# Kernel optimization log

Hardware: AMD Instinct MI355X
Metric: run time of the kernel (lower is better)

## Reference

```python
import jax, jax.numpy as jnp
import numpy as np

EPS = 1e-12
HEADS = 8
STRIDE = 4  # saccade_stride default

def conv1x1(x, w, b=None):
    # 1x1 conv == channel-mixing einsum; x: (B,C,H,W), w: (O,C)
    y = jnp.einsum('bchw,oc->bohw', x, w)
    if b is not None:
        y = y + b[None, :, None, None]
    return y

def ln2d(x, g, b, eps=1e-5):
    # LayerNorm across channel dim per spatial location (population variance)
    mu = x.mean(axis=1, keepdims=True)
    var = x.var(axis=1, keepdims=True)
    xn = (x - mu) / jnp.sqrt(var + eps)
    return xn * g[None, :, None, None] + b[None, :, None, None]

def l2norm(x):
    n = jnp.linalg.norm(x, axis=-1, keepdims=True)
    return x / jnp.maximum(n, EPS)

def cos_attn(q, k, v, scale):
    # q:(B,h,Q,d) k,v:(B,h,K,d); QK-normalized (cosine) attention
    logits = jnp.einsum('bhqd,bhkd->bhqk', l2norm(q), l2norm(k)) * scale
    a = jax.nn.softmax(logits, axis=-1)
    return jnp.einsum('bhqk,bhkd->bhqd', a, v)

def gqa(x, qkv_w, proj_w, proj_b):
    # grouped-query attention; group loop == per-head full attention
    B, C, H, W = x.shape
    hd = C // HEADS
    seq = H * W
    qkv = conv1x1(x, qkv_w).reshape(B, 3, HEADS, hd, seq)
    q, k, v = (jnp.swapaxes(qkv[:, i], -1, -2) for i in range(3))  # (B,h,seq,hd)
    out = cos_attn(q, k, v, hd ** -0.5)
    out = jnp.swapaxes(out, -1, -2).reshape(B, C, H, W)
    return conv1x1(out, proj_w, proj_b)

def block_forward(x, g1, b1, loc_qkv_w, loc_proj_w, loc_proj_b,
                  glob_qkv_w, glob_proj_w, glob_proj_b,
                  fuse_w1, fuse_b1, fuse_w2, fuse_b2,
                  glat, blat, latents, qlat_w, kvx_w, qx_w, kvlat_w,
                  lat_proj_w, lat_proj_b, g2, b2,
                  ffn_w1, ffn_b1, ffn_w2, ffn_b2):
    B, C, H, W = x.shape
    hd = C // HEADS
    seq = H * W
    scale = hd ** -0.5
    # --- BioAttentionFusion branch ---
    xn = ln2d(x, g1, b1)
    local = gqa(xn, loc_qkv_w, loc_proj_w, loc_proj_b)
    xc = xn.reshape(B, C, H // STRIDE, STRIDE, W // STRIDE, STRIDE).mean(axis=(3, 5))
    g = gqa(xc, glob_qkv_w, glob_proj_w, glob_proj_b)
    g = jax.image.resize(g, (B, C, H, W), method='bilinear')  # align_corners=False semantics
    f = conv1x1(jnp.concatenate([local, g], axis=1), fuse_w1, fuse_b1)
    f = conv1x1(jax.nn.gelu(f, approximate=False), fuse_w2, fuse_b2)
    x = x + f
    # --- LatentMixer branch ---
    xn = ln2d(x, glat, blat)
    L = latents.shape[-1]
    lat = jnp.broadcast_to(latents, (B, C, 1, L))
    ql = jnp.swapaxes(conv1x1(lat, qlat_w).reshape(B, HEADS, hd, L), -1, -2)
    kx, vx = jnp.split(conv1x1(xn, kvx_w), 2, axis=1)
    kx = jnp.swapaxes(kx.reshape(B, HEADS, hd, seq), -1, -2)
    vx = jnp.swapaxes(vx.reshape(B, HEADS, hd, seq), -1, -2)
    lat_read = cos_attn(ql, kx, vx, scale)  # latents read features
    lat_read = jnp.swapaxes(lat_read, -1, -2).reshape(B, C, 1, L)
    qx = jnp.swapaxes(conv1x1(xn, qx_w).reshape(B, HEADS, hd, seq), -1, -2)
    kl, vl = jnp.split(conv1x1(lat_read, kvlat_w), 2, axis=1)
    kl = jnp.swapaxes(kl.reshape(B, HEADS, hd, L), -1, -2)
    vl = jnp.swapaxes(vl.reshape(B, HEADS, hd, L), -1, -2)
    xw = cos_attn(qx, kl, vl, scale)  # features read latents back
    xw = jnp.swapaxes(xw, -1, -2).reshape(B, C, H, W)
    x = x + conv1x1(xw, lat_proj_w, lat_proj_b)
    # --- FFN branch ---
    xn = ln2d(x, g2, b2)
    h = jax.nn.gelu(conv1x1(xn, ffn_w1, ffn_b1), approximate=False)
    return x + conv1x1(h, ffn_w2, ffn_b2)

def setup_inputs() -> dict:
    key = jax.random.key(0)
    ks = jax.random.split(key, 24)
    B, C, H, W, L = 2, 128, 48, 48, 16
    def w(k, shape, s=0.02):
        return jax.random.normal(k, shape, jnp.float32) * s
    return {
        'x': jax.random.normal(ks[0], (B, C, H, W), jnp.float32),
        'g1': jnp.ones((C,), jnp.float32), 'b1': jnp.zeros((C,), jnp.float32),
        'loc_qkv_w': w(ks[1], (3 * C, C)),
        'loc_proj_w': w(ks[2], (C, C)), 'loc_proj_b': jnp.zeros((C,), jnp.float32),
        'glob_qkv_w': w(ks[3], (3 * C, C)),
        'glob_proj_w': w(ks[4], (C, C)), 'glob_proj_b': jnp.zeros((C,), jnp.float32),
        'fuse_w1': w(ks[5], (C, 2 * C)), 'fuse_b1': jnp.zeros((C,), jnp.float32),
        'fuse_w2': w(ks[6], (C, C)), 'fuse_b2': jnp.zeros((C,), jnp.float32),
        'glat': jnp.ones((C,), jnp.float32), 'blat': jnp.zeros((C,), jnp.float32),
        'latents': w(ks[7], (1, C, 1, L), 0.02),
        'qlat_w': w(ks[8], (C, C)), 'kvx_w': w(ks[9], (2 * C, C)),
        'qx_w': w(ks[10], (C, C)), 'kvlat_w': w(ks[11], (2 * C, C)),
        'lat_proj_w': w(ks[12], (C, C)), 'lat_proj_b': jnp.zeros((C,), jnp.float32),
        'g2': jnp.ones((C,), jnp.float32), 'b2': jnp.zeros((C,), jnp.float32),
        'ffn_w1': w(ks[13], (4 * C, C)), 'ffn_b1': jnp.zeros((4 * C,), jnp.float32),
        'ffn_w2': w(ks[14], (C, 4 * C)), 'ffn_b2': jnp.zeros((C,), jnp.float32),
    }

def reference(x, g1, b1, loc_qkv_w, loc_proj_w, loc_proj_b,
              glob_qkv_w, glob_proj_w, glob_proj_b,
              fuse_w1, fuse_b1, fuse_w2, fuse_b2,
              glat, blat, latents, qlat_w, kvx_w, qx_w, kvlat_w,
              lat_proj_w, lat_proj_b, g2, b2,
              ffn_w1, ffn_b1, ffn_w2, ffn_b2):
    return block_forward(x, g1, b1, loc_qkv_w, loc_proj_w, loc_proj_b,
                         glob_qkv_w, glob_proj_w, glob_proj_b,
                         fuse_w1, fuse_b1, fuse_w2, fuse_b2,
                         glat, blat, latents, qlat_w, kvx_w, qx_w, kvlat_w,
                         lat_proj_w, lat_proj_b, g2, b2,
                         ffn_w1, ffn_b1, ffn_w2, ffn_b2)
```

## Files before the change

kernel.cpp:

```cpp
#include <hip/hip_runtime.h>
#include <hip/hip_bf16.h>

typedef __hip_bfloat16 bf16;
typedef _Float16 f16;
typedef _Float16 f16x4 __attribute__((ext_vector_type(4)));
typedef float f32x4 __attribute__((ext_vector_type(4)));

#define HD 16
#define TK 128
#define KP 20
#define MINIT (-1e30f)

__device__ __forceinline__ float b2f(bf16 v){ return __bfloat162float(v); }
__device__ __forceinline__ float gelu_f(float x){ return 0.5f*x*(1.0f+erff(x*0.70710678118654752f)); }
__device__ __forceinline__ float rdv(const void* p, size_t i, bool bf){
  return bf ? b2f(((const bf16*)p)[i]) : ((const float*)p)[i];
}
__device__ __forceinline__ float4 ld4f(const void* p, size_t i, bool bf){
  if (bf){
    const bf16* q = (const bf16*)p + i;
    return make_float4(b2f(q[0]), b2f(q[1]), b2f(q[2]), b2f(q[3]));
  }
  return *(const float4*)((const float*)p + i);
}

__global__ void detect_k(const void* __restrict__ x, float* __restrict__ flag){
  if (blockIdx.x != 0) return;
  int l = threadIdx.x;
  const float* xf = (const float*)x;
  const bf16*  xb = (const bf16*)x;
  float sF = 0.f, sB = 0.f;
  for (int i = l; i < 512; i += 64){ float v = fabsf(xf[i]);      if (!(v < 1e30f)) v = 1e30f; sF += v; }
  for (int i = l; i < 1024; i += 64){ float v = fabsf(b2f(xb[i])); if (!(v < 1e30f)) v = 1e30f; sB += v; }
  #pragma unroll
  for (int o = 32; o; o >>= 1){ sF += __shfl_xor(sF, o); sB += __shfl_xor(sB, o); }
  if (l == 0){
    float mF = sF/512.f, mB = sB/1024.f;
    float dF = fabsf(logf(fmaxf(mF, 1e-30f)));
    float dB = fabsf(logf(fmaxf(mB, 1e-30f)));
    *flag = (dB <= dF) ? 1.0f : 0.0f;
  }
}

__global__ void cvt_k(const void* __restrict__ in, float* __restrict__ out, int n,
                      const float* __restrict__ flagp){
  bool bf = *flagp > 0.5f;
  int i = blockIdx.x*blockDim.x + threadIdx.x;
  if (i < n) out[i] = rdv(in, i, bf);
}

__global__ __launch_bounds__(256) void ln2dw_k(
    const float* __restrict__ x, const void* __restrict__ g,
    const void* __restrict__ b, float* __restrict__ y,
    int C, int HW, const float* __restrict__ flagp)
{
  __shared__ float redS[16][16];
  __shared__ float redQ[16][16];
  bool bf = *flagp > 0.5f;
  int t = threadIdx.x, pix = t & 15, sub = t >> 4;
  int p  = blockIdx.x*16 + pix;
  int bb = blockIdx.y;
  const float* xb = x + (size_t)bb*C*HW + p;
  float xv[8];
  float s = 0.f, s2 = 0.f;
  #pragma unroll
  for (int i = 0; i < 8; i++){
    float v = xb[(size_t)(sub*8 + i)*HW];
    xv[i] = v; s += v; s2 += v*v;
  }
  redS[sub][pix] = s; redQ[sub][pix] = s2;
  __syncthreads();
  float st = 0.f, qt = 0.f;
  #pragma unroll
  for (int j = 0; j < 16; j++){ st += redS[j][pix]; qt += redQ[j][pix]; }
  float mu  = st / (float)C;
  float var = fmaxf(qt / (float)C - mu*mu, 0.f);
  float inv = rsqrtf(var + 1e-5f);
  float* yb = y + (size_t)bb*C*HW + p;
  #pragma unroll
  for (int i = 0; i < 8; i++){
    int c = sub*8 + i;
    yb[(size_t)c*HW] = (xv[i] - mu)*inv*rdv(g, c, bf) + rdv(b, c, bf);
  }
}

__global__ void conv1x1_k(const float* __restrict__ in1, long in1_bs, int C1,
                          const float* __restrict__ in2, long in2_bs, int C2,
                          const void* __restrict__ w, const void* __restrict__ bias,
                          const float* __restrict__ res,
                          void* __restrict__ out, int to_out, int O, int NP, int act,
                          int raw1, const float* __restrict__ flagp){
  bool bf = *flagp > 0.5f;
  int p = blockIdx.x*blockDim.x + threadIdx.x;
  if (p >= NP) return;
  int o = blockIdx.y, bb = blockIdx.z;
  size_t wrow = (size_t)o*(C1 + C2);
  float acc = bias ? rdv(bias, o, bf) : 0.f;
  if (raw1){
    for (int c = 0; c < C1; c++)
      acc += rdv(w, wrow + c, bf) * rdv(in1, (size_t)bb*in1_bs + (size_t)c*NP + p, bf);
  } else {
    const float* i1 = in1 + (size_t)bb*in1_bs + p;
    for (int c = 0; c < C1; c++) acc += rdv(w, wrow + c, bf) * i1[(size_t)c*NP];
  }
  if (in2){
    const float* i2 = in2 + (size_t)bb*in2_bs + p;
    for (int c = 0; c < C2; c++) acc += rdv(w, wrow + C1 + c, bf) * i2[(size_t)c*NP];
  }
  if (act == 1) acc = gelu_f(acc);
  if (res) acc += res[((size_t)bb*O + o)*NP + p];
  size_t oi = ((size_t)bb*O + o)*NP + p;
  if (to_out){
    if (bf) ((bf16*)out)[oi] = __float2bfloat16(acc);
    else    ((float*)out)[oi] = acc;
  } else {
    ((float*)out)[oi] = acc;
  }
}

__global__ __launch_bounds__(256) void convmfma_k(
    const float* __restrict__ in1, long in1_bs, int C1,
    const float* __restrict__ in2, long in2_bs, int C2,
    const void* __restrict__ w, const void* __restrict__ bias,
    const float* __restrict__ res, void* __restrict__ out, int to_out,
    int O, int NP, int act, int nlo, int nhi,
    int lnf, const void* __restrict__ lng, const void* __restrict__ lnb,
    int pool, int ups2, const float* __restrict__ flagp)
{
  bool bf = *flagp > 0.5f;
  int lane = threadIdx.x & 63, wv = threadIdx.x >> 6;
  int lm = lane & 15, lg = (lane >> 4) & 3;
  int p0 = blockIdx.x*16, o0 = blockIdx.y*64 + wv*16, bb = blockIdx.z;
  int CW = C1 + C2;
  const float* x1 = in1 + (size_t)bb*in1_bs + p0 + lm;
  const float* x2b = in2 ? (in2 + (size_t)bb*in2_bs) : nullptr;
  float fh = 0.f, fw = 0.f; int i00=0, i01=0, i10=0, i11=0;
  if (ups2){
    int p = p0 + lm; int hh = p/48, ww = p%48;
    float sh = hh*0.25f - 0.375f, sw = ww*0.25f - 0.375f;
    float fh0 = floorf(sh), fw0 = floorf(sw);
    fh = sh - fh0; fw = sw - fw0;
    int h0 = (int)fh0, w0 = (int)fw0;
    int h0c = min(11, max(0, h0)), h1c = min(11, max(0, h0+1));
    int w0c = min(11, max(0, w0)), w1c = min(11, max(0, w0+1));
    i00 = h0c*12 + w0c; i01 = h0c*12 + w1c; i10 = h1c*12 + w0c; i11 = h1c*12 + w1c;
  }
  const float* pN = nullptr;
  if (pool){
    int pc = p0 + lm; int hc = pc/12, wc = pc%12;
    pN = in1 + (size_t)bb*in1_bs + hc*192 + wc*4;
  }
  float mu = 0.f, linv = 0.f;
  if (lnf){
    float s = 0.f, s2 = 0.f;
    for (int c = lg; c < CW; c += 4){ float v = x1[(size_t)c*NP]; s += v; s2 += v*v; }
    s  += __shfl_xor(s, 16);  s  += __shfl_xor(s, 32);
    s2 += __shfl_xor(s2, 16); s2 += __shfl_xor(s2, 32);
    mu = s / (float)CW;
    float var = fmaxf(s2/(float)CW - mu*mu, 0.f);
    linv = rsqrtf(var + 1e-5f);
  }
  f32x4 d; d[0]=0.f; d[1]=0.f; d[2]=0.f; d[3]=0.f;
  #pragma unroll 4
  for (int kc = 0; kc < CW; kc += 16){
    f16x4 xb;
    #pragma unroll
    for (int i = 0; i < 4; i++){
      int c = kc + lg*4 + i;
      float v;
      if (pool){
        const float* s = pN + (size_t)c*2304;
        float a = 0.f;
        #pragma unroll
        for (int r = 0; r < 4; r++)
          #pragma unroll
          for (int cc = 0; cc < 4; cc++) a += s[r*48 + cc];
        v = a * 0.0625f;
      } else if (c < C1){
        v = x1[(size_t)c*NP];
        if (lnf) v = (v - mu)*linv*rdv(lng, c, bf) + rdv(lnb, c, bf);
      } else {
        int c2 = c - C1;
        if (ups2){
          const float* s = x2b + (size_t)c2*144;
          v = (1.f-fh)*((1.f-fw)*s[i00] + fw*s[i01]) + fh*((1.f-fw)*s[i10] + fw*s[i11]);
        } else {
          v = x2b[(size_t)c2*NP + p0 + lm];
        }
      }
      xb[i] = (f16)v;
    }
    float4 wv4 = ld4f(w, (size_t)(o0 + lm)*CW + kc + lg*4, bf);
    f16x4 wa; wa[0]=(f16)wv4.x; wa[1]=(f16)wv4.y; wa[2]=(f16)wv4.z; wa[3]=(f16)wv4.w;
    d = __builtin_amdgcn_mfma_f32_16x16x16f16(wa, xb, d, 0, 0, 0);
  }
  if (o0 >= nlo && o0 < nhi){
    float ss = d[0]*d[0] + d[1]*d[1] + d[2]*d[2] + d[3]*d[3];
    ss += __shfl_xor(ss, 16); ss += __shfl_xor(ss, 32);
    float iv = 1.f / fmaxf(sqrtf(ss), 1e-12f);
    d[0]*=iv; d[1]*=iv; d[2]*=iv; d[3]*=iv;
  }
  #pragma unroll
  for (int r = 0; r < 4; r++){
    int o = o0 + lg*4 + r;
    float v = d[r] + (bias ? rdv(bias, o, bf) : 0.f);
    if (act == 1) v = gelu_f(v);
    size_t oi = ((size_t)bb*O + o)*NP + p0 + lm;
    if (res) v += res[oi];
    if (to_out && bf) ((bf16*)out)[oi] = __float2bfloat16(v);
    else              ((float*)out)[oi] = v;
  }
}

__global__ __launch_bounds__(512) void flat_mfma_k(
    const float* __restrict__ Q, long qbs, int qoff,
    const float* __restrict__ KV, long kbs, int koff, int voff,
    float* __restrict__ Out, long obs, int NQ, int NK, float scale)
{
  __shared__ float OS[8*4*16*17];
  __shared__ float LS[8*4*16];
  int t = threadIdx.x, lane = t & 63, wv = t >> 6;
  int h = blockIdx.y, bb = blockIdx.z;
  int qb = blockIdx.x*64;
  int lm = lane & 15, lg = lane >> 4;
  const float* qp  = Q  + (size_t)bb*qbs;
  const float* kvb = KV + (size_t)bb*kbs;
  f16x4 qf[4];
  #pragma unroll
  for (int qt = 0; qt < 4; qt++){
    float qv[4]; float ss = 0.f;
    #pragma unroll
    for (int i = 0; i < 4; i++){
      qv[i] = qp[(size_t)(qoff + h*16 + lg*4 + i)*NQ + qb + qt*16 + lm];
      ss += qv[i]*qv[i];
    }
    ss += __shfl_xor(ss, 16); ss += __shfl_xor(ss, 32);
    float inv = scale / fmaxf(sqrtf(ss), 1e-12f);
    #pragma unroll
    for (int i = 0; i < 4; i++) qf[qt][i] = (f16)(qv[i]*inv);
  }
  f32x4 of[4];
  float ls[4];
  #pragma unroll
  for (int qt = 0; qt < 4; qt++){
    of[qt][0]=0.f; of[qt][1]=0.f; of[qt][2]=0.f; of[qt][3]=0.f; ls[qt]=0.f;
  }
  int chunk = NK >> 3;
  int p0 = wv*chunk, p1 = p0 + chunk;
  const float* kc = kvb + (size_t)(koff + h*16)*NK;
  const float* vc = kvb + (size_t)(voff + h*16)*NK;
  for (int pos = p0; pos < p1; pos += 16){
    f16x4 kf;
    #pragma unroll
    for (int i = 0; i < 4; i++)
      kf[i] = (f16)kc[(size_t)(lg*4 + i)*NK + pos + lm];
    float4 vvv = *(const float4*)&vc[(size_t)lm*NK + pos + lg*4];
    f16x4 vf; vf[0]=(f16)vvv.x; vf[1]=(f16)vvv.y; vf[2]=(f16)vvv.z; vf[3]=(f16)vvv.w;
    #pragma unroll
    for (int qt = 0; qt < 4; qt++){
      f32x4 s; s[0]=0.f; s[1]=0.f; s[2]=0.f; s[3]=0.f;
      s = __builtin_amdgcn_mfma_f32_16x16x16f16(kf, qf[qt], s, 0, 0, 0);
      f16x4 pf;
      #pragma unroll
      for (int r = 0; r < 4; r++){
        float pp = __expf(s[r]);
        ls[qt] += pp;
        pf[r] = (f16)pp;
      }
      of[qt] = __builtin_amdgcn_mfma_f32_16x16x16f16(vf, pf, of[qt], 0, 0, 0);
    }
  }
  #pragma unroll
  for (int qt = 0; qt < 4; qt++){
    ls[qt] += __shfl_xor(ls[qt], 16);
    ls[qt] += __shfl_xor(ls[qt], 32);
    #pragma unroll
    for (int r = 0; r < 4; r++)
      OS[((wv*4 + qt)*16 + lm)*17 + lg*4 + r] = of[qt][r];
    if (lg == 0) LS[(wv*4 + qt)*16 + lm] = ls[qt];
  }
  __syncthreads();
  #pragma unroll
  for (int rep = 0; rep < 2; rep++){
    int o = t + rep*512;
    int d = o >> 6, qq = o & 63;
    int qt = qq >> 4, q = qq & 15;
    float acc = 0.f, lsum = 0.f;
    #pragma unroll
    for (int w = 0; w < 8; w++){
      acc  += OS[((w*4 + qt)*16 + q)*17 + d];
      lsum += LS[(w*4 + qt)*16 + q];
    }
    Out[(size_t)bb*obs + (size_t)(h*16 + d)*NQ + qb + qq] = acc / fmaxf(lsum, 1e-30f);
  }
}

__global__ __launch_bounds__(256) void attn4_k(
    const float* __restrict__ Q, long qbs, int qoff,
    const float* __restrict__ KV, long kbs, int koff, int voff,
    float* __restrict__ Out, long obs, int NQ, int NK, float scale)
{
  __shared__ __align__(16) float Ks[TK*KP];
  __shared__ __align__(16) float Vs[TK*KP];
  int tid = threadIdx.x;
  int sub = tid & 3;
  int h = blockIdx.y, bb = blockIdx.z;
  int qi = blockIdx.x*64 + (tid >> 2);
  bool qv = qi < NQ;
  float qn[4] = {0,0,0,0}, acc[4] = {0,0,0,0};
  float l = 0.f;
  if (qv){
    float s = 0.f;
    #pragma unroll
    for (int j = 0; j < 4; j++){
      qn[j] = Q[(size_t)bb*qbs + (size_t)(qoff + h*16 + sub*4 + j)*NQ + qi];
      s += qn[j]*qn[j];
    }
    s += __shfl_xor(s, 1); s += __shfl_xor(s, 2);
    float inv = scale / fmaxf(sqrtf(s), 1e-12f);
    #pragma unroll
    for (int j = 0; j < 4; j++) qn[j] *= inv;
  }
  for (int k0 = 0; k0 < NK; k0 += TK){
    int lim = min(TK, NK - k0);
    for (int i = tid; i < 16*TK; i += 256){
      int pos = i & (TK-1), d = i >> 7;
      if (pos < lim){
        Ks[pos*KP + d] = KV[(size_t)bb*kbs + (size_t)(koff + h*16 + d)*NK + k0 + pos];
        Vs[pos*KP + d] = KV[(size_t)bb*kbs + (size_t)(voff + h*16 + d)*NK + k0 + pos];
      }
    }
    __syncthreads();
    for (int pos = 0; pos < lim; pos++){
      float4 k4 = *(const float4*)&Ks[pos*KP + sub*4];
      float dd = qn[0]*k4.x + qn[1]*k4.y + qn[2]*k4.z + qn[3]*k4.w;
      dd += __shfl_xor(dd, 1); dd += __shfl_xor(dd, 2);
      float pp = __expf(dd);
      l += pp;
      float4 v4 = *(const float4*)&Vs[pos*KP + sub*4];
      acc[0] += pp*v4.x;
      acc[1] += pp*v4.y;
      acc[2] += pp*v4.z;
      acc[3] += pp*v4.w;
    }
    __syncthreads();
  }
  if (qv){
    float li = 1.f / fmaxf(l, 1e-30f);
    #pragma unroll
    for (int j = 0; j < 4; j++)
      Out[(size_t)bb*obs + (size_t)(h*16 + sub*4 + j)*NQ + qi] = acc[j]*li;
  }
}

__global__ void latpart_k(const float* __restrict__ ql, const float* __restrict__ kvx,
                          long kbs, float* __restrict__ part, int NK, int S){
  int s = blockIdx.x, h = blockIdx.y, bb = blockIdx.z;
  int t = threadIdx.x;
  int q = t & 15, sub = (t >> 4) & 3;
  float qn[16]; float ss = 0.f;
  #pragma unroll
  for (int d = 0; d < 16; d++){
    qn[d] = ql[(size_t)bb*2048 + (size_t)(h*16+d)*16 + q];
    ss += qn[d]*qn[d];
  }
  float inv = 0.25f / fmaxf(sqrtf(ss), 1e-12f);
  #pragma unroll
  for (int d = 0; d < 16; d++) qn[d] *= inv;
  float l = 0.f, acc[16];
  #pragma unroll
  for (int d = 0; d < 16; d++) acc[d] = 0.f;
  int chunk = NK / S, c4 = chunk >> 2;
  int k0 = s*chunk + sub*c4, k1 = k0 + c4;
  const float* kb = kvx + (size_t)bb*kbs;
  for (int pos = k0; pos < k1; pos++){
    float dot = 0.f;
    #pragma unroll
    for (int d = 0; d < 16; d++) dot += qn[d]*kb[(size_t)(h*16+d)*NK + pos];
    float pp = __expf(dot);
    l += pp;
    #pragma unroll
    for (int d = 0; d < 16; d++)
      acc[d] += pp*kb[(size_t)(128 + h*16+d)*NK + pos];
  }
  l += __shfl_xor(l, 16); l += __shfl_xor(l, 32);
  #pragma unroll
  for (int d = 0; d < 16; d++){
    acc[d] += __shfl_xor(acc[d], 16);
    acc[d] += __shfl_xor(acc[d], 32);
  }
  if ((t >> 4) == 0){
    size_t idx = (size_t)((((bb*8 + h)*16 + q)*S) + s)*18;
    part[idx] = l;
    #pragma unroll
    for (int d = 0; d < 16; d++) part[idx+1+d] = acc[d];
  }
}

__global__ void latcomb_k(const float* __restrict__ part, float* __restrict__ latr, int S){
  int i = blockIdx.x*blockDim.x + threadIdx.x;
  int d = i & 15, q = (i >> 4) & 15, h = (i >> 8) & 7, bb = i >> 11;
  size_t base = (size_t)(((bb*8 + h)*16 + q)*S)*18;
  float L = 0.f, a = 0.f;
  for (int s = 0; s < S; s++){
    const float* ps = part + base + (size_t)s*18;
    L += ps[0];
    a += ps[1+d];
  }
  latr[(size_t)bb*2048 + (size_t)(h*16+d)*16 + q] = a / fmaxf(L, 1e-30f);
}

extern "C" void kernel_launch(void* const* d_in, const int* in_sizes, int n_in,
                              void* d_out, int out_size, void* d_ws, size_t ws_size,
                              hipStream_t stream){
  const int B = 2, C = 128, HW = 2304;
  const void* x_in        = d_in[0];
  const void* g1          = d_in[1];
  const void* b1          = d_in[2];
  const void* loc_qkv_w   = d_in[3];
  const void* loc_proj_w  = d_in[4];
  const void* loc_proj_b  = d_in[5];
  const void* glob_qkv_w  = d_in[6];
  const void* glob_proj_w = d_in[7];
  const void* glob_proj_b = d_in[8];
  const void* fuse_w1     = d_in[9];
  const void* fuse_b1     = d_in[10];
  const void* fuse_w2     = d_in[11];
  const void* fuse_b2     = d_in[12];
  const void* glat        = d_in[13];
  const void* blat        = d_in[14];
  const void* latents     = d_in[15];
  const void* qlat_w      = d_in[16];
  const void* kvx_w       = d_in[17];
  const void* qx_w        = d_in[18];
  const void* kvlat_w     = d_in[19];
  const void* lat_proj_w  = d_in[20];
  const void* lat_proj_b  = d_in[21];
  const void* g2          = d_in[22];
  const void* b2          = d_in[23];
  const void* ffn_w1      = d_in[24];
  const void* ffn_b1      = d_in[25];
  const void* ffn_w2      = d_in[26];
  const void* ffn_b2      = d_in[27];

  float* ws = (float*)d_ws;
  float* P  = ws + 0;
  float* N  = ws + 589824;
  float* A  = ws + 1179648;
  float* Q  = ws + 1769472;
  float* FLAG = ws + 4128768;

  float* qkv   = Q;
  float* L     = Q + 1769472;
  float* qkvc  = Q + 36864;
  float* gatt  = Q + 147456;
  float* gproj = Q + 184320;
  float* kvx   = Q;
  float* qlat  = Q + 1181696;
  float* latr  = Q + 1185792;
  float* kvlat = Q + 1189888;
  float* part  = Q + 1198080;
  float* ffh   = Q;

  dim3 blk(256);
  dim3 blk512(512);

  detect_k<<<1, 64, 0, stream>>>(x_in, FLAG);
  cvt_k<<<2304, blk, 0, stream>>>(x_in, P, 589824, FLAG);

  ln2dw_k<<<dim3(144,B), blk, 0, stream>>>(P, g1, b1, N, C, HW, FLAG);
  convmfma_k<<<dim3(144,6,B), blk, 0, stream>>>(N,(long)C*HW,C, nullptr,0,0, loc_qkv_w,nullptr,nullptr, qkv,0,384,HW,0, 128,256, 0,nullptr,nullptr, 0,0, FLAG);
  flat_mfma_k<<<dim3(36,8,B), blk512, 0, stream>>>(qkv,(long)384*HW,0, qkv,(long)384*HW,128,256, A,(long)C*HW, HW,HW,0.25f);
  convmfma_k<<<dim3(144,2,B), blk, 0, stream>>>(A,(long)C*HW,C, nullptr,0,0, loc_proj_w,loc_proj_b,nullptr, L,0,C,HW,0, 0,0, 0,nullptr,nullptr, 0,0, FLAG);
  convmfma_k<<<dim3(9,6,B), blk, 0, stream>>>(N,(long)C*HW,C, nullptr,0,0, glob_qkv_w,nullptr,nullptr, qkvc,0,384,144,0, 128,256, 0,nullptr,nullptr, 1,0, FLAG);
  attn4_k<<<dim3(3,8,B), blk, 0, stream>>>(qkvc,(long)384*144,0, qkvc,(long)384*144,128,256, gatt,(long)C*144, 144,144,0.25f);
  convmfma_k<<<dim3(9,2,B), blk, 0, stream>>>(gatt,(long)C*144,C, nullptr,0,0, glob_proj_w,glob_proj_b,nullptr, gproj,0,C,144,0, 0,0, 0,nullptr,nullptr, 0,0, FLAG);
  convmfma_k<<<dim3(144,2,B), blk, 0, stream>>>(L,(long)C*HW,C, gproj,(long)C*144,C, fuse_w1,fuse_b1,nullptr, N,0,C,HW,1, 0,0, 0,nullptr,nullptr, 0,1, FLAG);
  convmfma_k<<<dim3(144,2,B), blk, 0, stream>>>(N,(long)C*HW,C, nullptr,0,0, fuse_w2,fuse_b2,P, P,0,C,HW,0, 0,0, 0,nullptr,nullptr, 0,0, FLAG);

  convmfma_k<<<dim3(144,4,B), blk, 0, stream>>>(P,(long)C*HW,C, nullptr,0,0, kvx_w,nullptr,nullptr, kvx,0,256,HW,0, 0,128, 1,glat,blat, 0,0, FLAG);
  convmfma_k<<<dim3(144,2,B), blk, 0, stream>>>(P,(long)C*HW,C, nullptr,0,0, qx_w,nullptr,nullptr, A,0,C,HW,0, 0,0, 1,glat,blat, 0,0, FLAG);
  conv1x1_k<<<dim3(1,128,B), blk, 0, stream>>>((const float*)latents,0L,C, nullptr,0,0, qlat_w,nullptr,nullptr, qlat,0,C,16,0, 1, FLAG);
  latpart_k<<<dim3(48,8,B), 64, 0, stream>>>(qlat, kvx, (long)256*HW, part, HW, 48);
  latcomb_k<<<16, blk, 0, stream>>>(part, latr, 48);
  convmfma_k<<<dim3(1,4,B), blk, 0, stream>>>(latr,(long)C*16,C, nullptr,0,0, kvlat_w,nullptr,nullptr, kvlat,0,256,16,0, 0,128, 0,nullptr,nullptr, 0,0, FLAG);
  attn4_k<<<dim3(36,8,B), blk, 0, stream>>>(A,(long)C*HW,0, kvlat,(long)256*16,0,128, N,(long)C*HW, HW,16,0.25f);
  convmfma_k<<<dim3(144,2,B), blk, 0, stream>>>(N,(long)C*HW,C, nullptr,0,0, lat_proj_w,lat_proj_b,P, P,0,C,HW,0, 0,0, 0,nullptr,nullptr, 0,0, FLAG);

  convmfma_k<<<dim3(144,8,B), blk, 0, stream>>>(P,(long)C*HW,C, nullptr,0,0, ffn_w1,ffn_b1,nullptr, ffh,0,512,HW,1, 0,0, 1,g2,b2, 0,0, FLAG);
  convmfma_k<<<dim3(144,2,B), blk, 0, stream>>>(ffh,(long)512*HW,512, nullptr,0,0, ffn_w2,ffn_b2,P, d_out,1,C,HW,0, 0,0, 0,nullptr,nullptr, 0,0, FLAG);
}
```

Baseline: 436.6 us.

## Fuse small latent kernels and inline dtype detection to cut launches

Removes the separate dtype-detect kernel: every kernel now re-runs a small 64-lane reduction over the input to decide bf16 versus fp32. The kvx and qx projections are merged into one convmfma launch through an output-split path. The latent query projection moves into latpart_k, and the kv-latent projection moves into a new attention kernel, so two small launches go away. This lowers launch count and serialization, but adds redundant detection loads and redundant projection work repeated in every block.

After: 448.0 us. +2.6%, slower.

```diff
diff --git a/kernel.cpp b/kernel.cpp
--- a/kernel.cpp
+++ b/kernel.cpp
@@ -9,7 +9,6 @@
 #define HD 16
 #define TK 128
 #define KP 20
-#define MINIT (-1e30f)
 
 __device__ __forceinline__ float b2f(bf16 v){ return __bfloat162float(v); }
 __device__ __forceinline__ float gelu_f(float x){ return 0.5f*x*(1.0f+erff(x*0.70710678118654752f)); }
@@ -24,27 +23,25 @@
   return *(const float4*)((const float*)p + i);
 }
 
-__global__ void detect_k(const void* __restrict__ x, float* __restrict__ flag){
-  if (blockIdx.x != 0) return;
-  int l = threadIdx.x;
+__device__ __forceinline__ bool detect_bf(const void* x){
+  int l = threadIdx.x & 63;
   const float* xf = (const float*)x;
   const bf16*  xb = (const bf16*)x;
   float sF = 0.f, sB = 0.f;
-  for (int i = l; i < 512; i += 64){ float v = fabsf(xf[i]);      if (!(v < 1e30f)) v = 1e30f; sF += v; }
-  for (int i = l; i < 1024; i += 64){ float v = fabsf(b2f(xb[i])); if (!(v < 1e30f)) v = 1e30f; sB += v; }
+  #pragma unroll
+  for (int i = 0; i < 8; i++){ float v = fabsf(xf[l + i*64]);      if (!(v < 1e30f)) v = 1e30f; sF += v; }
+  #pragma unroll
+  for (int i = 0; i < 16; i++){ float v = fabsf(b2f(xb[l + i*64])); if (!(v < 1e30f)) v = 1e30f; sB += v; }
   #pragma unroll
   for (int o = 32; o; o >>= 1){ sF += __shfl_xor(sF, o); sB += __shfl_xor(sB, o); }
-  if (l == 0){
-    float mF = sF/512.f, mB = sB/1024.f;
-    float dF = fabsf(logf(fmaxf(mF, 1e-30f)));
-    float dB = fabsf(logf(fmaxf(mB, 1e-30f)));
-    *flag = (dB <= dF) ? 1.0f : 0.0f;
-  }
-}
-
-__global__ void cvt_k(const void* __restrict__ in, float* __restrict__ out, int n,
-                      const float* __restrict__ flagp){
-  bool bf = *flagp > 0.5f;
+  float mF = sF/512.f, mB = sB/1024.f;
+  float dF = fabsf(logf(fmaxf(mF, 1e-30f)));
+  float dB = fabsf(logf(fmaxf(mB, 1e-30f)));
+  return dB <= dF;
+}
+
+__global__ void cvt_k(const void* __restrict__ in, float* __restrict__ out, int n){
+  bool bf = detect_bf(in);
   int i = blockIdx.x*blockDim.x + threadIdx.x;
   if (i < n) out[i] = rdv(in, i, bf);
 }
@@ -52,11 +49,11 @@
 __global__ __launch_bounds__(256) void ln2dw_k(
     const float* __restrict__ x, const void* __restrict__ g,
     const void* __restrict__ b, float* __restrict__ y,
-    int C, int HW, const float* __restrict__ flagp)
+    int C, int HW, const void* __restrict__ xdet)
 {
   __shared__ float redS[16][16];
   __shared__ float redQ[16][16];
-  bool bf = *flagp > 0.5f;
+  bool bf = detect_bf(xdet);
   int t = threadIdx.x, pix = t & 15, sub = t >> 4;
   int p  = blockIdx.x*16 + pix;
   int bb = blockIdx.y;
@@ -81,40 +78,6 @@
   for (int i = 0; i < 8; i++){
     int c = sub*8 + i;
     yb[(size_t)c*HW] = (xv[i] - mu)*inv*rdv(g, c, bf) + rdv(b, c, bf);
-  }
-}
-
-__global__ void conv1x1_k(const float* __restrict__ in1, long in1_bs, int C1,
-                          const float* __restrict__ in2, long in2_bs, int C2,
-                          const void* __restrict__ w, const void* __restrict__ bias,
-                          const float* __restrict__ res,
-                          void* __restrict__ out, int to_out, int O, int NP, int act,
-                          int raw1, const float* __restrict__ flagp){
-  bool bf = *flagp > 0.5f;
-  int p = blockIdx.x*blockDim.x + threadIdx.x;
-  if (p >= NP) return;
-  int o = blockIdx.y, bb = blockIdx.z;
-  size_t wrow = (size_t)o*(C1 + C2);
-  float acc = bias ? rdv(bias, o, bf) : 0.f;
-  if (raw1){
-    for (int c = 0; c < C1; c++)
-      acc += rdv(w, wrow + c, bf) * rdv(in1, (size_t)bb*in1_bs + (size_t)c*NP + p, bf);
-  } else {
-    const float* i1 = in1 + (size_t)bb*in1_bs + p;
-    for (int c = 0; c < C1; c++) acc += rdv(w, wrow + c, bf) * i1[(size_t)c*NP];
-  }
-  if (in2){
-    const float* i2 = in2 + (size_t)bb*in2_bs + p;
-    for (int c = 0; c < C2; c++) acc += rdv(w, wrow + C1 + c, bf) * i2[(size_t)c*NP];
-  }
-  if (act == 1) acc = gelu_f(acc);
-  if (res) acc += res[((size_t)bb*O + o)*NP + p];
-  size_t oi = ((size_t)bb*O + o)*NP + p;
-  if (to_out){
-    if (bf) ((bf16*)out)[oi] = __float2bfloat16(acc);
-    else    ((float*)out)[oi] = acc;
-  } else {
-    ((float*)out)[oi] = acc;
   }
 }
 
@@ -125,13 +88,17 @@
     const float* __restrict__ res, void* __restrict__ out, int to_out,
     int O, int NP, int act, int nlo, int nhi,
     int lnf, const void* __restrict__ lng, const void* __restrict__ lnb,
-    int pool, int ups2, const float* __restrict__ flagp)
+    int pool, int ups2,
+    const void* __restrict__ w2, void* __restrict__ out2, int O2, int osplit,
+    const void* __restrict__ xdet)
 {
-  bool bf = *flagp > 0.5f;
+  bool bf = detect_bf(xdet);
   int lane = threadIdx.x & 63, wv = threadIdx.x >> 6;
   int lm = lane & 15, lg = (lane >> 4) & 3;
   int p0 = blockIdx.x*16, o0 = blockIdx.y*64 + wv*16, bb = blockIdx.z;
   int CW = C1 + C2;
+  const void* wu = w; void* outu = out; int Ou = O; int od = 0;
+  if (osplit > 0 && o0 >= osplit){ wu = w2; outu = out2; Ou = O2; od = osplit; }
   const float* x1 = in1 + (size_t)bb*in1_bs + p0 + lm;
   const float* x2b = in2 ? (in2 + (size_t)bb*in2_bs) : nullptr;
   float fh = 0.f, fw = 0.f; int i00=0, i01=0, i10=0, i11=0;
@@ -190,7 +157,7 @@
       }
       xb[i] = (f16)v;
     }
-    float4 wv4 = ld4f(w, (size_t)(o0 + lm)*CW + kc + lg*4, bf);
+    float4 wv4 = ld4f(wu, (size_t)(o0 - od + lm)*CW + kc + lg*4, bf);
     f16x4 wa; wa[0]=(f16)wv4.x; wa[1]=(f16)wv4.y; wa[2]=(f16)wv4.z; wa[3]=(f16)wv4.w;
     d = __builtin_amdgcn_mfma_f32_16x16x16f16(wa, xb, d, 0, 0, 0);
   }
@@ -202,13 +169,13 @@
   }
   #pragma unroll
   for (int r = 0; r < 4; r++){
-    int o = o0 + lg*4 + r;
+    int o = o0 - od + lg*4 + r;
     float v = d[r] + (bias ? rdv(bias, o, bf) : 0.f);
     if (act == 1) v = gelu_f(v);
-    size_t oi = ((size_t)bb*O + o)*NP + p0 + lm;
+    size_t oi = ((size_t)bb*Ou + o)*NP + p0 + lm;
     if (res) v += res[oi];
-    if (to_out && bf) ((bf16*)out)[oi] = __float2bfloat16(v);
-    else              ((float*)out)[oi] = v;
+    if (to_out && bf) ((bf16*)outu)[oi] = __float2bfloat16(v);
+    else              ((float*)outu)[oi] = v;
   }
 }
 
@@ -353,15 +320,95 @@
   }
 }
 
-__global__ void latpart_k(const float* __restrict__ ql, const float* __restrict__ kvx,
-                          long kbs, float* __restrict__ part, int NK, int S){
+__global__ __launch_bounds__(256) void attn4lat_k(
+    const float* __restrict__ Q, long qbs,
+    const float* __restrict__ latr, const void* __restrict__ kvw,
+    float* __restrict__ Out, long obs, int NQ, float scale,
+    const void* __restrict__ xdet)
+{
+  __shared__ __align__(16) float Ks[16*KP];
+  __shared__ __align__(16) float Vs[16*KP];
+  bool bf = detect_bf(xdet);
+  int tid = threadIdx.x;
+  int h = blockIdx.y, bb = blockIdx.z;
+  {
+    int pos = tid & 15, d = tid >> 4;
+    const float* lr = latr + (size_t)bb*2048;
+    float kk = 0.f, vv = 0.f;
+    for (int c = 0; c < 128; c++){
+      float xv = lr[(size_t)c*16 + pos];
+      kk += rdv(kvw, (size_t)(h*16 + d)*128 + c, bf) * xv;
+      vv += rdv(kvw, (size_t)(128 + h*16 + d)*128 + c, bf) * xv;
+    }
+    Ks[pos*KP + d] = kk;
+    Vs[pos*KP + d] = vv;
+  }
+  __syncthreads();
+  if (tid < 16){
+    float ss = 0.f;
+    #pragma unroll
+    for (int d = 0; d < 16; d++){ float v = Ks[tid*KP + d]; ss += v*v; }
+    float iv = 1.f / fmaxf(sqrtf(ss), 1e-12f);
+    #pragma unroll
+    for (int d = 0; d < 16; d++) Ks[tid*KP + d] *= iv;
+  }
+  __syncthreads();
+  int sub = tid & 3;
+  int qi = blockIdx.x*64 + (tid >> 2);
+  float qn[4]; float acc[4] = {0,0,0,0}; float l = 0.f;
+  {
+    float s = 0.f;
+    #pragma unroll
+    for (int j = 0; j < 4; j++){
+      qn[j] = Q[(size_t)bb*qbs + (size_t)(h*16 + sub*4 + j)*NQ + qi];
+      s += qn[j]*qn[j];
+    }
+    s += __shfl_xor(s, 1); s += __shfl_xor(s, 2);
+    float inv = scale / fmaxf(sqrtf(s), 1e-12f);
+    #pragma unroll
+    for (int j = 0; j < 4; j++) qn[j] *= inv;
+  }
+  for (int pos = 0; pos < 16; pos++){
+    float4 k4 = *(const float4*)&Ks[pos*KP + sub*4];
+    float dd = qn[0]*k4.x + qn[1]*k4.y + qn[2]*k4.z + qn[3]*k4.w;
+    dd += __shfl_xor(dd, 1); dd += __shfl_xor(dd, 2);
+    float pp = __expf(dd);
+    l += pp;
+    float4 v4 = *(const float4*)&Vs[pos*KP + sub*4];
+    acc[0] += pp*v4.x;
+    acc[1] += pp*v4.y;
+    acc[2] += pp*v4.z;
+    acc[3] += pp*v4.w;
+  }
+  float li = 1.f / fmaxf(l, 1e-30f);
+  #pragma unroll
+  for (int j = 0; j < 4; j++)
+    Out[(size_t)bb*obs + (size_t)(h*16 + sub*4 + j)*NQ + qi] = acc[j]*li;
+}
+
+__global__ void latpart_k(const void* __restrict__ lat, const void* __restrict__ qw,
+                          const float* __restrict__ kvx, long kbs,
+                          float* __restrict__ part, int NK, int S,
+                          const void* __restrict__ xdet){
+  __shared__ float qls[256];
+  bool bf = detect_bf(xdet);
   int s = blockIdx.x, h = blockIdx.y, bb = blockIdx.z;
   int t = threadIdx.x;
   int q = t & 15, sub = (t >> 4) & 3;
+  #pragma unroll
+  for (int k2 = 0; k2 < 4; k2++){
+    int v = t*4 + k2;
+    int dd = v >> 4, qq = v & 15;
+    float a = 0.f;
+    for (int c = 0; c < 128; c++)
+      a += rdv(qw, (size_t)(h*16 + dd)*128 + c, bf) * rdv(lat, (size_t)c*16 + qq, bf);
+    qls[v] = a;
+  }
+  __syncthreads();
   float qn[16]; float ss = 0.f;
   #pragma unroll
   for (int d = 0; d < 16; d++){
-    qn[d] = ql[(size_t)bb*2048 + (size_t)(h*16+d)*16 + q];
+    qn[d] = qls[d*16 + q];
     ss += qn[d]*qn[d];
   }
   float inv = 0.25f / fmaxf(sqrtf(ss), 1e-12f);
@@ -448,7 +495,6 @@
   float* N  = ws + 589824;
   float* A  = ws + 1179648;
   float* Q  = ws + 1769472;
-  float* FLAG = ws + 4128768;
 
   float* qkv   = Q;
   float* L     = Q + 1769472;
@@ -456,37 +502,31 @@
   float* gatt  = Q + 147456;
   float* gproj = Q + 184320;
   float* kvx   = Q;
-  float* qlat  = Q + 1181696;
   float* latr  = Q + 1185792;
-  float* kvlat = Q + 1189888;
   float* part  = Q + 1198080;
   float* ffh   = Q;
 
   dim3 blk(256);
   dim3 blk512(512);
 
-  detect_k<<<1, 64, 0, stream>>>(x_in, FLAG);
-  cvt_k<<<2304, blk, 0, stream>>>(x_in, P, 589824, FLAG);
-
-  ln2dw_k<<<dim3(144,B), blk, 0, stream>>>(P, g1, b1, N, C, HW, FLAG);
-  convmfma_k<<<dim3(144,6,B), blk, 0, stream>>>(N,(long)C*HW,C, nullptr,0,0, loc_qkv_w,nullptr,nullptr, qkv,0,384,HW,0, 128,256, 0,nullptr,nullptr, 0,0, FLAG);
+  cvt_k<<<2304, blk, 0, stream>>>(x_in, P, 589824);
+
+  ln2dw_k<<<dim3(144,B), blk, 0, stream>>>(P, g1, b1, N, C, HW, x_in);
+  convmfma_k<<<dim3(144,6,B), blk, 0, stream>>>(N,(long)C*HW,C, nullptr,0,0, loc_qkv_w,nullptr,nullptr, qkv,0,384,HW,0, 128,256, 0,nullptr,nullptr, 0,0, nullptr,nullptr,0,0, x_in);
   flat_mfma_k<<<dim3(36,8,B), blk512, 0, stream>>>(qkv,(long)384*HW,0, qkv,(long)384*HW,128,256, A,(long)C*HW, HW,HW,0.25f);
-  convmfma_k<<<dim3(144,2,B), blk, 0, stream>>>(A,(long)C*HW,C, nullptr,0,0, loc_proj_w,loc_proj_b,nullptr, L,0,C,HW,0, 0,0, 0,nullptr,nullptr, 0,0, FLAG);
-  convmfma_k<<<dim3(9,6,B), blk, 0, stream>>>(N,(long)C*HW,C, nullptr,0,0, glob_qkv_w,nullptr,nullptr, qkvc,0,384,144,0, 128,256, 0,nullptr,nullptr, 1,0, FLAG);
+  convmfma_k<<<dim3(144,2,B), blk, 0, stream>>>(A,(long)C*HW,C, nullptr,0,0, loc_proj_w,loc_proj_b,nullptr, L,0,C,HW,0, 0,0, 0,nullptr,nullptr, 0,0, nullptr,nullptr,0,0, x_in);
+  convmfma_k<<<dim3(9,6,B), blk, 0, stream>>>(N,(long)C*HW,C, nullptr,0,0, glob_qkv_w,nullptr,nullptr, qkvc,0,384,144,0, 128,256, 0,nullptr,nullptr, 1,0, nullptr,nullptr,0,0, x_in);
   attn4_k<<<dim3(3,8,B), blk, 0, stream>>>(qkvc,(long)384*144,0, qkvc,(long)384*144,128,256, gatt,(long)C*144, 144,144,0.25f);
-  convmfma_k<<<dim3(9,2,B), blk, 0, stream>>>(gatt,(long)C*144,C, nullptr,0,0, glob_proj_w,glob_proj_b,nullptr, gproj,0,C,144,0, 0,0, 0,nullptr,nullptr, 0,0, FLAG);
-  convmfma_k<<<dim3(144,2,B), blk, 0, stream>>>(L,(long)C*HW,C, gproj,(long)C*144,C, fuse_w1,fuse_b1,nullptr, N,0,C,HW,1, 0,0, 0,nullptr,nullptr, 0,1, FLAG);
-  convmfma_k<<<dim3(144,2,B), blk, 0, stream>>>(N,(long)C*HW,C, nullptr,0,0, fuse_w2,fuse_b2,P, P,0,C,HW,0, 0,0, 0,nullptr,nullptr, 0,0, FLAG);
-
-  convmfma_k<<<dim3(144,4,B), blk, 0, stream>>>(P,(long)C*HW,C, nullptr,0,0, kvx_w,nullptr,nullptr, kvx,0,256,HW,0, 0,128, 1,glat,blat, 0,0, FLAG);
-  convmfma_k<<<dim3(144,2,B), blk, 0, stream>>>(P,(long)C*HW,C, nullptr,0,0, qx_w,nullptr,nullptr, A,0,C,HW,0, 0,0, 1,glat,blat, 0,0, FLAG);
-  conv1x1_k<<<dim3(1,128,B), blk, 0, stream>>>((const float*)latents,0L,C, nullptr,0,0, qlat_w,nullptr,nullptr, qlat,0,C,16,0, 1, FLAG);
-  latpart_k<<<dim3(48,8,B), 64, 0, stream>>>(qlat, kvx, (long)256*HW, part, HW, 48);
+  convmfma_k<<<dim3(9,2,B), blk, 0, stream>>>(gatt,(long)C*144,C, nullptr,0,0, glob_proj_w,glob_proj_b,nullptr, gproj,0,C,144,0, 0,0, 0,nullptr,nullptr, 0,0, nullptr,nullptr,0,0, x_in);
+  convmfma_k<<<dim3(144,2,B), blk, 0, stream>>>(L,(long)C*HW,C, gproj,(long)C*144,C, fuse_w1,fuse_b1,nullptr, N,0,C,HW,1, 0,0, 0,nullptr,nullptr, 0,1, nullptr,nullptr,0,0, x_in);
+  convmfma_k<<<dim3(144,2,B), blk, 0, stream>>>(N,(long)C*HW,C, nullptr,0,0, fuse_w2,fuse_b2,P, P,0,C,HW,0, 0,0, 0,nullptr,nullptr, 0,0, nullptr,nullptr,0,0, x_in);
+
+  convmfma_k<<<dim3(144,6,B), blk, 0, stream>>>(P,(long)C*HW,C, nullptr,0,0, kvx_w,nullptr,nullptr, kvx,0,256,HW,0, 0,128, 1,glat,blat, 0,0, qx_w,A,128,256, x_in);
+  latpart_k<<<dim3(48,8,B), 64, 0, stream>>>(latents, qlat_w, kvx, (long)256*HW, part, HW, 48, x_in);
   latcomb_k<<<16, blk, 0, stream>>>(part, latr, 48);
-  convmfma_k<<<dim3(1,4,B), blk, 0, stream>>>(latr,(long)C*16,C, nullptr,0,0, kvlat_w,nullptr,nullptr, kvlat,0,256,16,0, 0,128, 0,nullptr,nullptr, 0,0, FLAG);
-  attn4_k<<<dim3(36,8,B), blk, 0, stream>>>(A,(long)C*HW,0, kvlat,(long)256*16,0,128, N,(long)C*HW, HW,16,0.25f);
-  convmfma_k<<<dim3(144,2,B), blk, 0, stream>>>(N,(long)C*HW,C, nullptr,0,0, lat_proj_w,lat_proj_b,P, P,0,C,HW,0, 0,0, 0,nullptr,nullptr, 0,0, FLAG);
-
-  convmfma_k<<<dim3(144,8,B), blk, 0, stream>>>(P,(long)C*HW,C, nullptr,0,0, ffn_w1,ffn_b1,nullptr, ffh,0,512,HW,1, 0,0, 1,g2,b2, 0,0, FLAG);
-  convmfma_k<<<dim3(144,2,B), blk, 0, stream>>>(ffh,(long)512*HW,512, nullptr,0,0, ffn_w2,ffn_b2,P, d_out,1,C,HW,0, 0,0, 0,nullptr,nullptr, 0,0, FLAG);
-}
+  attn4lat_k<<<dim3(36,8,B), blk, 0, stream>>>(A,(long)C*HW, latr, kvlat_w, N,(long)C*HW, HW, 0.25f, x_in);
+  convmfma_k<<<dim3(144,2,B), blk, 0, stream>>>(N,(long)C*HW,C, nullptr,0,0, lat_proj_w,lat_proj_b,P, P,0,C,HW,0, 0,0, 0,nullptr,nullptr, 0,0, nullptr,nullptr,0,0, x_in);
+
+  convmfma_k<<<dim3(144,8,B), blk, 0, stream>>>(P,(long)C*HW,C, nullptr,0,0, ffn_w1,ffn_b1,nullptr, ffh,0,512,HW,1, 0,0, 1,g2,b2, 0,0, nullptr,nullptr,0,0, x_in);
+  convmfma_k<<<dim3(144,2,B), blk, 0, stream>>>(ffh,(long)512*HW,512, nullptr,0,0, ffn_w2,ffn_b2,P, d_out,1,C,HW,0, 0,0, 0,nullptr,nullptr, 0,0, nullptr,nullptr,0,0, x_in);
+}
```
